# Kernel optimization log

Hardware: AMD Instinct MI355X
Metric: run time of the kernel (lower is better)

## Reference

```python
import jax, jax.numpy as jnp
import numpy as np
from jax import lax

# ---- configuration (mirrors YOLOF init kwargs) ----
B = 32            # batch
H = W = 64        # single-level feature map (stride 32)
NA = 6            # anchors per location
A = H * W * NA    # 24576 total anchors
C = 80            # num_classes
K = 1000          # test_topk_candidates
MAXDET = 100      # max_detections_per_image
SCORE_TH = 0.05   # test_score_thresh
NMS_TH = 0.6      # test_nms_thresh
STRIDE = 32
ANCHOR_SIZES = (32.0, 64.0, 96.0, 128.0, 256.0, 512.0)
SCALE_CLAMP = float(np.log(1000.0 / 16))  # detectron2 Box2BoxTransform clamp
CLS_OFFSET = 1e4  # coordinate offset for class-aware NMS


def _make_anchors() -> np.ndarray:
    ys, xs = np.meshgrid(np.arange(H), np.arange(W), indexing='ij')
    cx = (xs.astype(np.float32) + 0.5) * STRIDE  # [H,W]
    cy = (ys.astype(np.float32) + 0.5) * STRIDE
    sizes = np.asarray(ANCHOR_SIZES, np.float32)  # [NA]
    half = sizes / 2.0
    x1 = cx[..., None] - half; y1 = cy[..., None] - half
    x2 = cx[..., None] + half; y2 = cy[..., None] + half
    return np.stack([x1, y1, x2, y2], axis=-1).reshape(A, 4)


def setup_inputs() -> dict:
    key = jax.random.key(0)
    k1, k2 = jax.random.split(key)
    pred_logits = jax.random.normal(k1, (B, A, C), dtype=jnp.float32)
    pred_deltas = jax.random.normal(k2, (B, A, 4), dtype=jnp.float32) * 0.1
    anchors = jnp.asarray(_make_anchors())
    return {"pred_logits": pred_logits, "pred_deltas": pred_deltas, "anchors": anchors}


def _apply_deltas(deltas, boxes):
    """detectron2 Box2BoxTransform.apply_deltas, weights (1,1,1,1). deltas/boxes: [N,4]."""
    w = boxes[:, 2] - boxes[:, 0]
    h = boxes[:, 3] - boxes[:, 1]
    cx = boxes[:, 0] + 0.5 * w
    cy = boxes[:, 1] + 0.5 * h
    dx, dy, dw, dh = deltas[:, 0], deltas[:, 1], deltas[:, 2], deltas[:, 3]
    dw = jnp.minimum(dw, SCALE_CLAMP)
    dh = jnp.minimum(dh, SCALE_CLAMP)
    pcx = dx * w + cx
    pcy = dy * h + cy
    pw = jnp.exp(dw) * w
    ph = jnp.exp(dh) * h
    return jnp.stack([pcx - 0.5 * pw, pcy - 0.5 * ph, pcx + 0.5 * pw, pcy + 0.5 * ph], axis=-1)


def _iou_one_vs_all(box, boxes):
    """IoU of box [4] against boxes [K,4]."""
    lt = jnp.maximum(box[:2], boxes[:, :2])
    rb = jnp.minimum(box[2:], boxes[:, 2:])
    wh = jnp.clip(rb - lt, 0.0)
    inter = wh[:, 0] * wh[:, 1]
    area1 = (box[2] - box[0]) * (box[3] - box[1])
    area2 = (boxes[:, 2] - boxes[:, 0]) * (boxes[:, 3] - boxes[:, 1])
    return inter / (area1 + area2 - inter + 1e-9)


def _greedy_nms(boxes, valid):
    """boxes [K,4] sorted by score desc; valid [K] bool. Returns kept mask [K]."""
    idx = jnp.arange(K)
    def body(i, carry):
        suppressed, kept = carry
        alive = jnp.logical_not(suppressed[i])
        ious = _iou_one_vs_all(lax.stop_gradient(boxes[i]), lax.stop_gradient(boxes))
        supp_new = suppressed | (alive & (ious > NMS_TH) & (idx > i))
        kept = kept.at[i].set(alive)
        return (supp_new, kept)
    suppressed0 = jnp.logical_not(valid)
    kept0 = jnp.zeros((K,), dtype=bool)
    _, kept = lax.fori_loop(0, K, body, (suppressed0, kept0))
    return kept & valid


def _process_image(logits, deltas, anchors):
    # logits [A,C], deltas [A,4]
    scores = jax.nn.sigmoid(logits).reshape(A * C)
    top_scores, top_idx = lax.top_k(scores, K)          # sorted desc
    anchor_idx = top_idx // C
    cls_idx = top_idx % C
    valid = top_scores > SCORE_TH
    boxes = _apply_deltas(deltas[anchor_idx], anchors[anchor_idx])  # [K,4]
    # class-aware NMS via per-class coordinate offset
    nms_boxes = boxes + cls_idx.astype(boxes.dtype)[:, None] * CLS_OFFSET
    kept = _greedy_nms(nms_boxes, valid)
    kept_scores = jnp.where(kept, top_scores, 0.0)
    det_scores, det_i = lax.top_k(kept_scores, MAXDET)
    det_boxes = boxes[det_i]            # [MAXDET,4]
    det_cls = cls_idx[det_i]            # [MAXDET]
    det = jnp.concatenate([det_boxes, det_scores[:, None]], axis=-1)  # [MAXDET,5]
    return det, det_cls


def reference(pred_logits, pred_deltas, anchors):
    det, det_cls = jax.vmap(_process_image, in_axes=(0, 0, None))(pred_logits, pred_deltas, anchors)
    return det, det_cls  # [B,100,5] float (x1,y1,x2,y2,score), [B,100] int classes
```

## Files before the change

kernel.cpp:

```cpp
#include <hip/hip_runtime.h>

typedef unsigned long long u64;
typedef unsigned int u32;

#define DEV static __device__ __forceinline__

constexpr int NB   = 32;
constexpr int NA_  = 24576;
constexpr int NC   = 80;
constexpr int AC   = NA_ * NC;
constexpr int KTOP = 1000;
constexpr int NDET = 100;
constexpr int CAND_CAP = 16384;
constexpr int SEL_CAP  = 2048;
constexpr float CUT = 2.5f;

constexpr int BLOCKS_PER_IMG = 96;
constexpr int F4_PER_IMG   = AC / 4;
constexpr int F4_PER_BLOCK = F4_PER_IMG / BLOCKS_PER_IMG;
constexpr int LCAP = 1024;
constexpr int CNT_PAD = 32;

__device__ int   g_cnt[NB * CNT_PAD];
__device__ int   g_hist[NB][1024];
__device__ u64   g_cand[NB][CAND_CAP];
__device__ float g_boxes[NB][1024][4];
__device__ float g_nbox[NB][1024][4];
__device__ float g_scores[NB][1024];
__device__ int   g_cls[NB][1024];
__device__ u64   g_invalid[NB][16];
__device__ u64   g_mask[NB][1024][16];
__device__ u64   g_keptw[NB][16];

DEV float exp_cr(float x) { return (float)exp((double)x); }
DEV float sigmoid_np(float x) {
    float ef = exp_cr(-x);
    return __fdiv_rn(1.0f, __fadd_rn(1.0f, ef));
}

DEV u64 shfl_u64(u64 x, int src) {
    int lo = __shfl((int)(u32)(x & 0xffffffffULL), src, 64);
    int hi = __shfl((int)(u32)(x >> 32), src, 64);
    return ((u64)(u32)hi << 32) | (u32)lo;
}

__global__ void k0_init() {
    int t = blockIdx.x * blockDim.x + threadIdx.x;
    if (t < NB * CNT_PAD) g_cnt[t] = 0;
    if (t < NB * 1024) ((int*)g_hist)[t] = 0;
}

__global__ void __launch_bounds__(256) k1_scan(const float* __restrict__ logits) {
    __shared__ u64 lc[LCAP];
    __shared__ int lcnt;
    __shared__ int gbase;
    const int blk = blockIdx.x;
    const int b = blk / BLOCKS_PER_IMG;
    const int c = blk - b * BLOCKS_PER_IMG;
    if (threadIdx.x == 0) lcnt = 0;
    __syncthreads();

    const float4* src = reinterpret_cast<const float4*>(logits)
                        + (size_t)b * F4_PER_IMG + (size_t)c * F4_PER_BLOCK;
    const u32 base_idx = (u32)c * (u32)F4_PER_BLOCK * 4u;
#pragma unroll 4
    for (int i = 0; i < F4_PER_BLOCK / 256; ++i) {
        int t = i * 256 + threadIdx.x;
        float4 v = src[t];
        u32 e0 = base_idx + (u32)t * 4u;
        float vals[4] = {v.x, v.y, v.z, v.w};
#pragma unroll
        for (int q = 0; q < 4; ++q) {
            if (vals[q] > CUT) {
                u32 key = __float_as_uint(vals[q]);
                int pos = atomicAdd(&lcnt, 1);
                if (pos < LCAP) lc[pos] = ((u64)key << 32) | (e0 + q);
                int bin = (int)((key - 0x40000000u) >> 14);
                if (bin > 1023) bin = 1023;
                atomicAdd(&g_hist[b][bin], 1);
            }
        }
    }
    __syncthreads();
    const int n = min(lcnt, LCAP);
    if (threadIdx.x == 0) gbase = atomicAdd(&g_cnt[b * CNT_PAD], n);
    __syncthreads();
    const int gb = gbase;
    for (int t = threadIdx.x; t < n; t += 256) {
        int p = gb + t;
        if (p < CAND_CAP) g_cand[b][p] = lc[t];
    }
}

__global__ void __launch_bounds__(1024) k3_select(const float* __restrict__ deltas,
                                                  const float* __restrict__ anchors) {
    const int b = blockIdx.x;
    const int tid = threadIdx.x;
    __shared__ u64 arr[SEL_CAP];
    __shared__ int sT, s_cnt;

    if (tid == 0) {
        int cum = 0, T = 0;
        for (int bin = 1023; bin >= 0; --bin) {
            cum += g_hist[b][bin];
            if (cum >= KTOP) { T = bin; break; }
        }
        sT = (T > 0) ? T - 1 : 0;
        s_cnt = 0;
    }
    arr[tid] = 0ULL;
    arr[tid + 1024] = 0ULL;
    __syncthreads();

    const int cnt = min(g_cnt[b * CNT_PAD], CAND_CAP);
    const int Tm1 = sT;
    for (int t = tid; t < cnt; t += 1024) {
        u64 c = g_cand[b][t];
        u32 key = (u32)(c >> 32);
        int bin = (int)((key - 0x40000000u) >> 14);
        if (bin > 1023) bin = 1023;
        if (bin >= Tm1) {
            float logit = __uint_as_float(key);
            float score = sigmoid_np(logit);
            u32 idx = (u32)c;
            u64 comp = ((u64)__float_as_uint(score) << 32) | (u32)(~idx);
            int p = atomicAdd(&s_cnt, 1);
            if (p < SEL_CAP) arr[p] = comp;
        }
    }
    __syncthreads();

    for (int k = 2; k <= SEL_CAP; k <<= 1) {
        for (int j = k >> 1; j > 0; j >>= 1) {
            for (int i = tid; i < SEL_CAP; i += 1024) {
                int ixj = i ^ j;
                if (ixj > i) {
                    bool dir = (i & k) == 0;
                    u64 x = arr[i], y = arr[ixj];
                    if ((x < y) == dir) { arr[i] = y; arr[ixj] = x; }
                }
            }
            __syncthreads();
        }
    }

    bool valid = false;
    {
        int t = tid;
        if (t < KTOP) {
            u64 c = arr[t];
            if (c != 0ULL) {
                u32 sb = (u32)(c >> 32);
                float score = __uint_as_float(sb);
                u32 idx = ~((u32)c);
                int anchor = (int)(idx / NC);
                int cls = (int)(idx - (u32)anchor * NC);
                const float* dp = deltas + ((size_t)b * NA_ + anchor) * 4;
                const float* ap = anchors + (size_t)anchor * 4;
                float ax = ap[0], ay = ap[1], az = ap[2], aw = ap[3];
                float w = __fsub_rn(az, ax);
                float h = __fsub_rn(aw, ay);
                float cx = __fadd_rn(ax, __fmul_rn(0.5f, w));
                float cy = __fadd_rn(ay, __fmul_rn(0.5f, h));
                float ddx = dp[0], ddy = dp[1], ddw = dp[2], ddh = dp[3];
                const float SC = (float)4.135166556742356;
                ddw = fminf(ddw, SC);
                ddh = fminf(ddh, SC);
                float pcx = __fadd_rn(__fmul_rn(ddx, w), cx);
                float pcy = __fadd_rn(__fmul_rn(ddy, h), cy);
                float pw = __fmul_rn(exp_cr(ddw), w);
                float ph = __fmul_rn(exp_cr(ddh), h);
                float hx = __fmul_rn(0.5f, pw);
                float hy = __fmul_rn(0.5f, ph);
                float bx0 = __fsub_rn(pcx, hx), by0 = __fsub_rn(pcy, hy);
                float bx1 = __fadd_rn(pcx, hx), by1 = __fadd_rn(pcy, hy);
                g_boxes[b][t][0] = bx0; g_boxes[b][t][1] = by0;
                g_boxes[b][t][2] = bx1; g_boxes[b][t][3] = by1;
                float off = __fmul_rn((float)cls, 10000.0f);
                g_nbox[b][t][0] = __fadd_rn(bx0, off);
                g_nbox[b][t][1] = __fadd_rn(by0, off);
                g_nbox[b][t][2] = __fadd_rn(bx1, off);
                g_nbox[b][t][3] = __fadd_rn(by1, off);
                g_scores[b][t] = score;
                g_cls[b][t] = cls;
                valid = score > 0.05f;
            }
        }
    }
    u64 bal = __ballot(!valid);
    if ((tid & 63) == 0) g_invalid[b][tid >> 6] = bal;
}

__global__ void k4_mask() {
    int gw = blockIdx.x * 4 + (threadIdx.x >> 6);
    int lane = threadIdx.x & 63;
    if (gw >= NB * KTOP) return;
    int b = gw / KTOP;
    int i = gw - b * KTOP;
    float ax = g_nbox[b][i][0], ay = g_nbox[b][i][1], az = g_nbox[b][i][2], aw = g_nbox[b][i][3];
    float a1 = __fmul_rn(__fsub_rn(az, ax), __fsub_rn(aw, ay));
#pragma unroll 4
    for (int w = 0; w < 16; ++w) {
        u64 m = 0ULL;
        if (((w << 6) + 63) > i) {
            int j = (w << 6) + lane;
            bool cond = (j > i) && (j < KTOP);
            if (cond) {
                const float* bj = g_nbox[b][j];
                float bx = bj[0], by = bj[1], bz = bj[2], bw = bj[3];
                float ltx = fmaxf(ax, bx), lty = fmaxf(ay, by);
                float rbx = fminf(az, bz), rby = fminf(aw, bw);
                float wx = fmaxf(__fsub_rn(rbx, ltx), 0.0f);
                float wy = fmaxf(__fsub_rn(rby, lty), 0.0f);
                float inter = __fmul_rn(wx, wy);
                float a2 = __fmul_rn(__fsub_rn(bz, bx), __fsub_rn(bw, by));
                float den = __fadd_rn(__fsub_rn(__fadd_rn(a1, a2), inter), 1e-9f);
                float iou = __fdiv_rn(inter, den);
                cond = iou > 0.6f;
            }
            m = __ballot(cond);
        }
        if (lane == 0) g_mask[b][i][w] = m;
    }
}

__global__ void __launch_bounds__(64) k5_nms() {
    const int b = blockIdx.x;
    const int lane = threadIdx.x;
    u64 own = (lane < 16) ? g_invalid[b][lane] : 0ULL;
    u64 pf_own[16], pf_row[16];
#pragma unroll
    for (int k = 0; k < 16; ++k) {
        pf_own[k] = (lane < 16) ? g_mask[b][k][lane] : 0ULL;
        pf_row[k] = g_mask[b][k][0];
    }
    for (int wb = 0; wb < 16; ++wb) {
        u64 live = shfl_u64(own, wb);
        u64 kw = 0ULL;
#pragma unroll
        for (int sub = 0; sub < 4; ++sub) {
#pragma unroll
            for (int k = 0; k < 16; ++k) {
                int i = wb * 64 + sub * 16 + k;
                bool alive = ((live >> (i & 63)) & 1ULL) == 0ULL;
                u64 rw = pf_row[k];
                u64 ow = pf_own[k];
                if (alive) {
                    live |= rw;
                    if (lane < 16) own |= ow;
                    kw |= 1ULL << (i & 63);
                }
                int ni = i + 16; if (ni > 1023) ni = 1023;
                pf_own[k] = (lane < 16) ? g_mask[b][ni][lane] : 0ULL;
                pf_row[k] = g_mask[b][ni][ni >> 6];
            }
        }
        if (lane == 0) g_keptw[b][wb] = kw;
    }
}

__global__ void __launch_bounds__(1024) k6_out(float* __restrict__ out) {
    const int b = blockIdx.x;
    const int t = threadIdx.x;
    bool kept = false;
    if (t < KTOP) kept = ((g_keptw[b][t >> 6] >> (t & 63)) & 1ULL) != 0ULL;
    int ks = kept ? 1 : 0;
    __shared__ int s[1024];
    __shared__ int snk;
    s[t] = ks;
    __syncthreads();
    for (int off = 1; off < 1024; off <<= 1) {
        int add = (t >= off) ? s[t - off] : 0;
        __syncthreads();
        s[t] += add;
        __syncthreads();
    }
    if (t == 1023) snk = s[1023];
    __syncthreads();
    const int nkept = snk;
    if (t < KTOP) {
        int excl = s[t] - ks;
        int p;
        float sc;
        if (kept) { p = excl; sc = g_scores[b][t]; }
        else      { p = nkept + (t - excl); sc = 0.0f; }
        if (p < NDET) {
            float* det = out + ((size_t)b * NDET + p) * 5;
            det[0] = g_boxes[b][t][0];
            det[1] = g_boxes[b][t][1];
            det[2] = g_boxes[b][t][2];
            det[3] = g_boxes[b][t][3];
            det[4] = sc;
            out[(size_t)NB * NDET * 5 + (size_t)b * NDET + p] = (float)g_cls[b][t];
        }
    }
}

extern "C" void kernel_launch(void* const* d_in, const int* in_sizes, int n_in,
                              void* d_out, int out_size, void* d_ws, size_t ws_size,
                              hipStream_t stream) {
    const float* logits  = (const float*)d_in[0];
    const float* deltas  = (const float*)d_in[1];
    const float* anchors = (const float*)d_in[2];
    float* out = (float*)d_out;

    k0_init<<<128, 256, 0, stream>>>();
    k1_scan<<<NB * BLOCKS_PER_IMG, 256, 0, stream>>>(logits);
    k3_select<<<NB, 1024, 0, stream>>>(deltas, anchors);
    k4_mask<<<(NB * KTOP) / 4, 256, 0, stream>>>();
    k5_nms<<<NB, 64, 0, stream>>>();
    k6_out<<<NB, 1024, 0, stream>>>(out);
}
```

Baseline: 557.8 us.

## Fuse select, IoU mask, NMS and output into one per-image kernel

The select, IoU-mask, greedy-NMS and output kernels are merged into a single 1024-thread block per image. Boxes, scores, the invalid mask and the kept mask now live in shared memory instead of global arrays. The separate init kernel is removed: each image's histogram and counter are reset after they are read. The threshold search over the histogram becomes a parallel suffix scan instead of a serial loop. This cuts kernel launches and global round trips, but the IoU mask is now computed by only 32 blocks rather than spread across the whole GPU.

```diff
diff --git a/kernel.cpp b/kernel.cpp
--- a/kernel.cpp
+++ b/kernel.cpp
@@ -24,13 +24,7 @@
 __device__ int   g_cnt[NB * CNT_PAD];
 __device__ int   g_hist[NB][1024];
 __device__ u64   g_cand[NB][CAND_CAP];
-__device__ float g_boxes[NB][1024][4];
-__device__ float g_nbox[NB][1024][4];
-__device__ float g_scores[NB][1024];
-__device__ int   g_cls[NB][1024];
-__device__ u64   g_invalid[NB][16];
 __device__ u64   g_mask[NB][1024][16];
-__device__ u64   g_keptw[NB][16];
 
 DEV float exp_cr(float x) { return (float)exp((double)x); }
 DEV float sigmoid_np(float x) {
@@ -42,12 +36,6 @@
     int lo = __shfl((int)(u32)(x & 0xffffffffULL), src, 64);
     int hi = __shfl((int)(u32)(x >> 32), src, 64);
     return ((u64)(u32)hi << 32) | (u32)lo;
-}
-
-__global__ void k0_init() {
-    int t = blockIdx.x * blockDim.x + threadIdx.x;
-    if (t < NB * CNT_PAD) g_cnt[t] = 0;
-    if (t < NB * 1024) ((int*)g_hist)[t] = 0;
 }
 
 __global__ void __launch_bounds__(256) k1_scan(const float* __restrict__ logits) {
@@ -92,27 +80,44 @@
     }
 }
 
-__global__ void __launch_bounds__(1024) k3_select(const float* __restrict__ deltas,
-                                                  const float* __restrict__ anchors) {
+__global__ void __launch_bounds__(1024) k2_fused(const float* __restrict__ deltas,
+                                                 const float* __restrict__ anchors,
+                                                 float* __restrict__ out) {
     const int b = blockIdx.x;
     const int tid = threadIdx.x;
-    __shared__ u64 arr[SEL_CAP];
-    __shared__ int sT, s_cnt;
-
+    __shared__ u64   arr[SEL_CAP];
+    __shared__ float snbox[KTOP * 5 + 8];
+    __shared__ float sbox[KTOP * 4];
+    __shared__ int   sscan[1024];
+    __shared__ u64   sinv[16], skept[16];
+    __shared__ int   sT, s_cnt, s_gcnt, s_nk;
+
+    sscan[tid] = g_hist[b][tid];
+    g_hist[b][tid] = 0;
     if (tid == 0) {
-        int cum = 0, T = 0;
-        for (int bin = 1023; bin >= 0; --bin) {
-            cum += g_hist[b][bin];
-            if (cum >= KTOP) { T = bin; break; }
-        }
-        sT = (T > 0) ? T - 1 : 0;
+        s_gcnt = min(g_cnt[b * CNT_PAD], CAND_CAP);
+        g_cnt[b * CNT_PAD] = 0;
         s_cnt = 0;
+        sT = 0;
     }
     arr[tid] = 0ULL;
     arr[tid + 1024] = 0ULL;
     __syncthreads();
 
-    const int cnt = min(g_cnt[b * CNT_PAD], CAND_CAP);
+    for (int off = 1; off < 1024; off <<= 1) {
+        int v = (tid + off < 1024) ? sscan[tid + off] : 0;
+        __syncthreads();
+        sscan[tid] += v;
+        __syncthreads();
+    }
+    {
+        int suf = sscan[tid];
+        if (suf >= KTOP && (tid == 1023 || sscan[tid + 1] < KTOP))
+            sT = (tid > 0) ? tid - 1 : 0;
+    }
+    __syncthreads();
+
+    const int cnt = s_gcnt;
     const int Tm1 = sT;
     for (int t = tid; t < cnt; t += 1024) {
         u64 c = g_cand[b][t];
@@ -120,10 +125,8 @@
         int bin = (int)((key - 0x40000000u) >> 14);
         if (bin > 1023) bin = 1023;
         if (bin >= Tm1) {
-            float logit = __uint_as_float(key);
-            float score = sigmoid_np(logit);
-            u32 idx = (u32)c;
-            u64 comp = ((u64)__float_as_uint(score) << 32) | (u32)(~idx);
+            float score = sigmoid_np(__uint_as_float(key));
+            u64 comp = ((u64)__float_as_uint(score) << 32) | (u32)(~(u32)c);
             int p = atomicAdd(&s_cnt, 1);
             if (p < SEL_CAP) arr[p] = comp;
         }
@@ -145,153 +148,150 @@
     }
 
     bool valid = false;
+    if (tid < KTOP) {
+        u64 c = arr[tid];
+        if (c != 0ULL) {
+            float score = __uint_as_float((u32)(c >> 32));
+            u32 idx = ~((u32)c);
+            int anchor = (int)(idx / NC);
+            int cls = (int)(idx - (u32)anchor * NC);
+            const float* dp = deltas + ((size_t)b * NA_ + anchor) * 4;
+            const float* ap = anchors + (size_t)anchor * 4;
+            float ax = ap[0], ay = ap[1], az = ap[2], aw = ap[3];
+            float w = __fsub_rn(az, ax);
+            float h = __fsub_rn(aw, ay);
+            float cx = __fadd_rn(ax, __fmul_rn(0.5f, w));
+            float cy = __fadd_rn(ay, __fmul_rn(0.5f, h));
+            float ddx = dp[0], ddy = dp[1], ddw = dp[2], ddh = dp[3];
+            const float SC = (float)4.135166556742356;
+            ddw = fminf(ddw, SC);
+            ddh = fminf(ddh, SC);
+            float pcx = __fadd_rn(__fmul_rn(ddx, w), cx);
+            float pcy = __fadd_rn(__fmul_rn(ddy, h), cy);
+            float pw = __fmul_rn(exp_cr(ddw), w);
+            float ph = __fmul_rn(exp_cr(ddh), h);
+            float hx = __fmul_rn(0.5f, pw);
+            float hy = __fmul_rn(0.5f, ph);
+            float bx0 = __fsub_rn(pcx, hx), by0 = __fsub_rn(pcy, hy);
+            float bx1 = __fadd_rn(pcx, hx), by1 = __fadd_rn(pcy, hy);
+            sbox[tid * 4 + 0] = bx0; sbox[tid * 4 + 1] = by0;
+            sbox[tid * 4 + 2] = bx1; sbox[tid * 4 + 3] = by1;
+            float off = __fmul_rn((float)cls, 10000.0f);
+            snbox[tid * 5 + 0] = __fadd_rn(bx0, off);
+            snbox[tid * 5 + 1] = __fadd_rn(by0, off);
+            snbox[tid * 5 + 2] = __fadd_rn(bx1, off);
+            snbox[tid * 5 + 3] = __fadd_rn(by1, off);
+            valid = score > 0.05f;
+        } else {
+            sbox[tid * 4 + 0] = 0.f; sbox[tid * 4 + 1] = 0.f;
+            sbox[tid * 4 + 2] = 0.f; sbox[tid * 4 + 3] = 0.f;
+            snbox[tid * 5 + 0] = 0.f; snbox[tid * 5 + 1] = 0.f;
+            snbox[tid * 5 + 2] = 0.f; snbox[tid * 5 + 3] = 0.f;
+        }
+    }
     {
-        int t = tid;
-        if (t < KTOP) {
-            u64 c = arr[t];
-            if (c != 0ULL) {
-                u32 sb = (u32)(c >> 32);
-                float score = __uint_as_float(sb);
-                u32 idx = ~((u32)c);
-                int anchor = (int)(idx / NC);
-                int cls = (int)(idx - (u32)anchor * NC);
-                const float* dp = deltas + ((size_t)b * NA_ + anchor) * 4;
-                const float* ap = anchors + (size_t)anchor * 4;
-                float ax = ap[0], ay = ap[1], az = ap[2], aw = ap[3];
-                float w = __fsub_rn(az, ax);
-                float h = __fsub_rn(aw, ay);
-                float cx = __fadd_rn(ax, __fmul_rn(0.5f, w));
-                float cy = __fadd_rn(ay, __fmul_rn(0.5f, h));
-                float ddx = dp[0], ddy = dp[1], ddw = dp[2], ddh = dp[3];
-                const float SC = (float)4.135166556742356;
-                ddw = fminf(ddw, SC);
-                ddh = fminf(ddh, SC);
-                float pcx = __fadd_rn(__fmul_rn(ddx, w), cx);
-                float pcy = __fadd_rn(__fmul_rn(ddy, h), cy);
-                float pw = __fmul_rn(exp_cr(ddw), w);
-                float ph = __fmul_rn(exp_cr(ddh), h);
-                float hx = __fmul_rn(0.5f, pw);
-                float hy = __fmul_rn(0.5f, ph);
-                float bx0 = __fsub_rn(pcx, hx), by0 = __fsub_rn(pcy, hy);
-                float bx1 = __fadd_rn(pcx, hx), by1 = __fadd_rn(pcy, hy);
-                g_boxes[b][t][0] = bx0; g_boxes[b][t][1] = by0;
-                g_boxes[b][t][2] = bx1; g_boxes[b][t][3] = by1;
-                float off = __fmul_rn((float)cls, 10000.0f);
-                g_nbox[b][t][0] = __fadd_rn(bx0, off);
-                g_nbox[b][t][1] = __fadd_rn(by0, off);
-                g_nbox[b][t][2] = __fadd_rn(bx1, off);
-                g_nbox[b][t][3] = __fadd_rn(by1, off);
-                g_scores[b][t] = score;
-                g_cls[b][t] = cls;
-                valid = score > 0.05f;
-            }
-        }
-    }
-    u64 bal = __ballot(!valid);
-    if ((tid & 63) == 0) g_invalid[b][tid >> 6] = bal;
-}
-
-__global__ void k4_mask() {
-    int gw = blockIdx.x * 4 + (threadIdx.x >> 6);
-    int lane = threadIdx.x & 63;
-    if (gw >= NB * KTOP) return;
-    int b = gw / KTOP;
-    int i = gw - b * KTOP;
-    float ax = g_nbox[b][i][0], ay = g_nbox[b][i][1], az = g_nbox[b][i][2], aw = g_nbox[b][i][3];
-    float a1 = __fmul_rn(__fsub_rn(az, ax), __fsub_rn(aw, ay));
-#pragma unroll 4
-    for (int w = 0; w < 16; ++w) {
-        u64 m = 0ULL;
-        if (((w << 6) + 63) > i) {
-            int j = (w << 6) + lane;
-            bool cond = (j > i) && (j < KTOP);
-            if (cond) {
-                const float* bj = g_nbox[b][j];
-                float bx = bj[0], by = bj[1], bz = bj[2], bw = bj[3];
-                float ltx = fmaxf(ax, bx), lty = fmaxf(ay, by);
-                float rbx = fminf(az, bz), rby = fminf(aw, bw);
-                float wx = fmaxf(__fsub_rn(rbx, ltx), 0.0f);
-                float wy = fmaxf(__fsub_rn(rby, lty), 0.0f);
-                float inter = __fmul_rn(wx, wy);
-                float a2 = __fmul_rn(__fsub_rn(bz, bx), __fsub_rn(bw, by));
-                float den = __fadd_rn(__fsub_rn(__fadd_rn(a1, a2), inter), 1e-9f);
-                float iou = __fdiv_rn(inter, den);
-                cond = iou > 0.6f;
-            }
-            m = __ballot(cond);
-        }
-        if (lane == 0) g_mask[b][i][w] = m;
-    }
-}
-
-__global__ void __launch_bounds__(64) k5_nms() {
-    const int b = blockIdx.x;
-    const int lane = threadIdx.x;
-    u64 own = (lane < 16) ? g_invalid[b][lane] : 0ULL;
-    u64 pf_own[16], pf_row[16];
+        u64 bal = __ballot(!valid);
+        if ((tid & 63) == 0) sinv[tid >> 6] = bal;
+    }
+    __syncthreads();
+
+    {
+        int wv = tid >> 6, lane = tid & 63;
+        for (int i = wv; i < 1024; i += 16) {
+            float ax = 0.f, ay = 0.f, az = 0.f, aw = 0.f;
+            if (i < KTOP) {
+                ax = snbox[i * 5 + 0]; ay = snbox[i * 5 + 1];
+                az = snbox[i * 5 + 2]; aw = snbox[i * 5 + 3];
+            }
+            float a1 = __fmul_rn(__fsub_rn(az, ax), __fsub_rn(aw, ay));
+            for (int w = i >> 6; w < 16; ++w) {
+                int j = (w << 6) + lane;
+                bool cond = (j > i) && (j < KTOP);
+                if (cond) {
+                    float bx = snbox[j * 5 + 0], by = snbox[j * 5 + 1];
+                    float bz = snbox[j * 5 + 2], bw = snbox[j * 5 + 3];
+                    float ltx = fmaxf(ax, bx), lty = fmaxf(ay, by);
+                    float rbx = fminf(az, bz), rby = fminf(aw, bw);
+                    float wx = fmaxf(__fsub_rn(rbx, ltx), 0.0f);
+                    float wy = fmaxf(__fsub_rn(rby, lty), 0.0f);
+                    float inter = __fmul_rn(wx, wy);
+                    float a2 = __fmul_rn(__fsub_rn(bz, bx), __fsub_rn(bw, by));
+                    float den = __fadd_rn(__fsub_rn(__fadd_rn(a1, a2), inter), 1e-9f);
+                    float iou = __fdiv_rn(inter, den);
+                    cond = iou > 0.6f;
+                }
+                u64 m = __ballot(cond);
+                if (lane == 0) g_mask[b][i][w] = m;
+            }
+        }
+    }
+    __syncthreads();
+
+    if (tid < 64) {
+        int lane = tid;
+        u64 own = (lane < 16) ? sinv[lane] : 0ULL;
+        u64 pf_own[8], pf_row[8];
 #pragma unroll
-    for (int k = 0; k < 16; ++k) {
-        pf_own[k] = (lane < 16) ? g_mask[b][k][lane] : 0ULL;
-        pf_row[k] = g_mask[b][k][0];
-    }
-    for (int wb = 0; wb < 16; ++wb) {
-        u64 live = shfl_u64(own, wb);
-        u64 kw = 0ULL;
+        for (int k = 0; k < 8; ++k) {
+            pf_own[k] = (lane < 16) ? g_mask[b][k][lane] : 0ULL;
+            pf_row[k] = g_mask[b][k][0];
+        }
+        for (int wb = 0; wb < 16; ++wb) {
+            u64 live = shfl_u64(own, wb);
+            u64 kw = 0ULL;
+            for (int sub = 0; sub < 8; ++sub) {
 #pragma unroll
-        for (int sub = 0; sub < 4; ++sub) {
-#pragma unroll
-            for (int k = 0; k < 16; ++k) {
-                int i = wb * 64 + sub * 16 + k;
-                bool alive = ((live >> (i & 63)) & 1ULL) == 0ULL;
-                u64 rw = pf_row[k];
-                u64 ow = pf_own[k];
-                if (alive) {
-                    live |= rw;
-                    if (lane < 16) own |= ow;
-                    kw |= 1ULL << (i & 63);
+                for (int k = 0; k < 8; ++k) {
+                    int i = wb * 64 + sub * 8 + k;
+                    bool alive = ((live >> (i & 63)) & 1ULL) == 0ULL;
+                    u64 rw = pf_row[k];
+                    u64 ow = pf_own[k];
+                    if (alive) {
+                        live |= rw;
+                        if (lane < 16) own |= ow;
+                        kw |= 1ULL << (i & 63);
+                    }
+                    int ni = i + 8; if (ni > 1023) ni = 1023;
+                    pf_own[k] = (lane < 16) ? g_mask[b][ni][lane] : 0ULL;
+                    pf_row[k] = g_mask[b][ni][ni >> 6];
                 }
-                int ni = i + 16; if (ni > 1023) ni = 1023;
-                pf_own[k] = (lane < 16) ? g_mask[b][ni][lane] : 0ULL;
-                pf_row[k] = g_mask[b][ni][ni >> 6];
-            }
-        }
-        if (lane == 0) g_keptw[b][wb] = kw;
-    }
-}
-
-__global__ void __launch_bounds__(1024) k6_out(float* __restrict__ out) {
-    const int b = blockIdx.x;
-    const int t = threadIdx.x;
+            }
+            if (lane == 0) skept[wb] = kw;
+        }
+    }
+    __syncthreads();
+
     bool kept = false;
-    if (t < KTOP) kept = ((g_keptw[b][t >> 6] >> (t & 63)) & 1ULL) != 0ULL;
+    if (tid < KTOP) kept = ((skept[tid >> 6] >> (tid & 63)) & 1ULL) != 0ULL;
     int ks = kept ? 1 : 0;
-    __shared__ int s[1024];
-    __shared__ int snk;
-    s[t] = ks;
+    sscan[tid] = ks;
     __syncthreads();
     for (int off = 1; off < 1024; off <<= 1) {
-        int add = (t >= off) ? s[t - off] : 0;
+        int add = (tid >= off) ? sscan[tid - off] : 0;
         __syncthreads();
-        s[t] += add;
+        sscan[tid] += add;
         __syncthreads();
     }
-    if (t == 1023) snk = s[1023];
-    __syncthreads();
-    const int nkept = snk;
-    if (t < KTOP) {
-        int excl = s[t] - ks;
-        int p;
-        float sc;
-        if (kept) { p = excl; sc = g_scores[b][t]; }
-        else      { p = nkept + (t - excl); sc = 0.0f; }
+    if (tid == 1023) s_nk = sscan[1023];
+    __syncthreads();
+    const int nkept = s_nk;
+    if (tid < KTOP) {
+        int excl = sscan[tid] - ks;
+        u64 c = arr[tid];
+        int p; float sc;
+        if (kept) { p = excl; sc = __uint_as_float((u32)(c >> 32)); }
+        else      { p = nkept + (tid - excl); sc = 0.0f; }
         if (p < NDET) {
             float* det = out + ((size_t)b * NDET + p) * 5;
-            det[0] = g_boxes[b][t][0];
-            det[1] = g_boxes[b][t][1];
-            det[2] = g_boxes[b][t][2];
-            det[3] = g_boxes[b][t][3];
+            det[0] = sbox[tid * 4 + 0];
+            det[1] = sbox[tid * 4 + 1];
+            det[2] = sbox[tid * 4 + 2];
+            det[3] = sbox[tid * 4 + 3];
             det[4] = sc;
-            out[(size_t)NB * NDET * 5 + (size_t)b * NDET + p] = (float)g_cls[b][t];
+            u32 idx = ~((u32)c);
+            int anchor = (int)(idx / NC);
+            int cls = (int)(idx - (u32)anchor * NC);
+            out[(size_t)NB * NDET * 5 + (size_t)b * NDET + p] = (float)cls;
         }
     }
 }
@@ -304,10 +304,6 @@
     const float* anchors = (const float*)d_in[2];
     float* out = (float*)d_out;
 
-    k0_init<<<128, 256, 0, stream>>>();
     k1_scan<<<NB * BLOCKS_PER_IMG, 256, 0, stream>>>(logits);
-    k3_select<<<NB, 1024, 0, stream>>>(deltas, anchors);
-    k4_mask<<<(NB * KTOP) / 4, 256, 0, stream>>>();
-    k5_nms<<<NB, 64, 0, stream>>>();
-    k6_out<<<NB, 1024, 0, stream>>>(out);
-}
+    k2_fused<<<NB, 1024, 0, stream>>>(deltas, anchors, out);
+}
```

Result: slower. 652.9 us (+17.1%).
